# Kernel optimization log

Measured on AMD Instinct MI355X. Metric: run time of the kernel, lower is better.

The kernel has to match this reference:

```python
import jax, jax.numpy as jnp
import numpy as np

N = 50000      # nodes
E = 800000     # edges (before self-loops)
IN = 256       # input_dim
HID = 72       # hidden_dim
HEADS = 4
NEG_SLOPE = 0.2  # PyG GATConv default leaky-relu slope


def setup_inputs() -> dict:
    key = jax.random.key(0)
    ks = jax.random.split(key, 16)
    rn = lambda k, shape: jax.random.normal(k, shape, jnp.float32) * 0.05
    return {
        "x": jax.random.normal(ks[0], (N, IN), jnp.float32),
        "edge_index": jax.random.randint(ks[1], (2, E), 0, N),
        "W_in": rn(ks[2], (IN, HID)), "b_in": jnp.zeros((HID,), jnp.float32),
        "W1": rn(ks[3], (HID, HEADS * HID)),
        "a_src1": rn(ks[4], (HEADS, HID)), "a_dst1": rn(ks[5], (HEADS, HID)),
        "b1": jnp.zeros((HEADS * HID,), jnp.float32),
        "W2": rn(ks[6], (HEADS * HID, HID)),
        "a_src2": rn(ks[7], (1, HID)), "a_dst2": rn(ks[8], (1, HID)),
        "b2": jnp.zeros((HID,), jnp.float32),
        "W3": rn(ks[9], (HID, HID)),
        "a_src3": rn(ks[10], (1, HID)), "a_dst3": rn(ks[11], (1, HID)),
        "b3": jnp.zeros((HID,), jnp.float32),
        "Ws1": rn(ks[12], (HID, 32)), "bs1": jnp.zeros((32,), jnp.float32),
        "Ws2": rn(ks[13], (32, 1)), "bs2": jnp.zeros((1,), jnp.float32),
    }


def gat_conv(x, src, dst, W, a_src, a_dst, bias, concat):
    # PyG GATConv (eval mode): per-head linear, leaky-relu attention logits,
    # segment softmax over incoming edges per destination, scatter-aggregate.
    H, C = a_src.shape
    h = (x @ W).reshape(-1, H, C)                      # [N, H, C]
    logit_s = jnp.einsum('nhc,hc->nh', h, a_src)       # [N, H]
    logit_d = jnp.einsum('nhc,hc->nh', h, a_dst)       # [N, H]
    e = jax.nn.leaky_relu(logit_s[src] + logit_d[dst], NEG_SLOPE)   # [Et, H]
    emax = jax.ops.segment_max(e, dst, num_segments=N)
    emax = jnp.where(jnp.isfinite(emax), emax, 0.0)
    p = jnp.exp(e - emax[dst])
    denom = jax.ops.segment_sum(p, dst, num_segments=N)
    alpha = p / jnp.maximum(denom[dst], 1e-16)         # [Et, H]
    out = jax.ops.segment_sum(h[src] * alpha[:, :, None], dst, num_segments=N)
    out = out.reshape(-1, H * C) if concat else out.mean(axis=1)
    return out + bias


def reference(x, edge_index, W_in, b_in,
              W1, a_src1, a_dst1, b1,
              W2, a_src2, a_dst2, b2,
              W3, a_src3, a_dst3, b3,
              Ws1, bs1, Ws2, bs2):
    loops = jnp.arange(N)                              # PyG add_self_loops=True
    src = jnp.concatenate([edge_index[0], loops])
    dst = jnp.concatenate([edge_index[1], loops])
    x0 = x @ W_in + b_in                               # [N, HID]
    h = jax.nn.elu(gat_conv(x0, src, dst, W1, a_src1, a_dst1, b1, True))
    h = jax.nn.elu(gat_conv(h, src, dst, W2, a_src2, a_dst2, b2, False))
    h = jax.nn.elu(gat_conv(h, src, dst, W3, a_src3, a_dst3, b3, False))
    h = h + x0
    score = jax.nn.relu(h @ Ws1 + bs1) @ Ws2 + bs2     # dropout = identity (eval)
    return score.squeeze(-1)                           # [N]
```

## Files before the change

kernel.cpp:

```cpp
#include <hip/hip_runtime.h>
#include <hip/hip_fp16.h>
#include <cmath>

#define NN 50000
#define EE 800000
#define ET (EE + NN)
#define IN_DIM 256
#define HID 72
#define CAP 96

typedef __attribute__((ext_vector_type(8))) short s8v;
typedef __attribute__((ext_vector_type(4))) short s4v;
typedef __attribute__((ext_vector_type(4))) float f4v;
typedef __attribute__((ext_vector_type(2))) float f2v;

__device__ __forceinline__ ushort f2bf(float x) {
    uint u = __float_as_uint(x);
    return (ushort)((u + 0x7fffu + ((u >> 16) & 1u)) >> 16);
}
__device__ __forceinline__ float bf2f(ushort h) {
    return __uint_as_float(((uint)h) << 16);
}
__device__ __forceinline__ void split4(const float4& v, s4v& h, s4v& l) {
    ushort h0 = f2bf(v.x), h1 = f2bf(v.y), h2 = f2bf(v.z), h3 = f2bf(v.w);
    h = (s4v){(short)h0, (short)h1, (short)h2, (short)h3};
    l = (s4v){(short)f2bf(v.x - bf2f(h0)), (short)f2bf(v.y - bf2f(h1)),
              (short)f2bf(v.z - bf2f(h2)), (short)f2bf(v.w - bf2f(h3))};
}
__device__ __forceinline__ f4v mfma16(s8v a, s8v b, f4v c) {
    return __builtin_amdgcn_mfma_f32_16x16x32_bf16(a, b, c, 0, 0, 0);
}
__device__ __forceinline__ f2v unpack_h2(uint pv) {
    __half2 hv = __builtin_bit_cast(__half2, pv);
    return (f2v){__low2float(hv), __high2float(hv)};
}
__device__ __forceinline__ uint pack_h2(float a, float b) {
    __half2 hp = __floats2half2_rn(a, b);
    return __builtin_bit_cast(uint, hp);
}
__device__ __forceinline__ f2v fma2(float w, f2v c, f2v a) {
    return __builtin_elementwise_fma((f2v){w, w}, c, a);
}
__device__ __forceinline__ void unpack_split8(uint4 u, s8v& ah, s8v& al) {
    f2v p0 = unpack_h2(u.x), p1 = unpack_h2(u.y);
    f2v p2 = unpack_h2(u.z), p3 = unpack_h2(u.w);
    float x[8] = {p0.x, p0.y, p1.x, p1.y, p2.x, p2.y, p3.x, p3.y};
    #pragma unroll
    for (int i = 0; i < 8; ++i) {
        ushort hi = f2bf(x[i]);
        ah[i] = (short)hi;
        al[i] = (short)f2bf(x[i] - bf2f(hi));
    }
}

__device__ __forceinline__ void wsplit_one(const float* W, int ldw, int K,
        int idx, short* outH, short* outL) {
    int h = idx / (72 * K);
    int rem = idx - h * 72 * K;
    int n = rem / K, k = rem - n * K;
    float v = W[(size_t)k * ldw + h * 72 + n];
    ushort hi = f2bf(v);
    outH[idx] = (short)hi;
    outL[idx] = (short)f2bf(v - bf2f(hi));
}

#define PR0 18432
#define PR1 (PR0 + 20736)
#define PR2 (PR1 + 20736)
#define PR3 (PR2 + 5184)
#define PR4 (PR3 + 288)
#define PRTOT (PR4 + NN)

__global__ __launch_bounds__(256) void prep_kernel(
        const float* __restrict__ W_in, const float* __restrict__ W1,
        const float* __restrict__ W2, const float* __restrict__ W3,
        const float* __restrict__ a_src, const float* __restrict__ a_dst,
        short* __restrict__ BtInH, short* __restrict__ BtInL,
        short* __restrict__ Bt1H, short* __restrict__ Bt1L,
        short* __restrict__ Bt2H, short* __restrict__ Bt2L,
        short* __restrict__ Bt3H, short* __restrict__ Bt3L,
        float* __restrict__ wsrc, float* __restrict__ wdst,
        int* __restrict__ deg, ushort* __restrict__ ell) {
    int gid = blockIdx.x * 256 + threadIdx.x;
    if (gid < PR0) {
        wsplit_one(W_in, 72, 256, gid, BtInH, BtInL);
    } else if (gid < PR1) {
        wsplit_one(W1, 288, 72, gid - PR0, Bt1H, Bt1L);
    } else if (gid < PR2) {
        wsplit_one(W2, 72, 288, gid - PR1, Bt2H, Bt2L);
    } else if (gid < PR3) {
        wsplit_one(W3, 72, 72, gid - PR2, Bt3H, Bt3L);
    } else if (gid < PR4) {
        int j = gid - PR3;
        int h = j / HID, k = j % HID;
        const float* wrow = W1 + (size_t)k * (4 * HID) + h * HID;
        const float* as = a_src + h * HID;
        const float* ad = a_dst + h * HID;
        float s = 0.f, d = 0.f;
        for (int c = 0; c < HID; ++c) {
            float w = wrow[c];
            s = fmaf(w, as[c], s);
            d = fmaf(w, ad[c], d);
        }
        wsrc[j] = s;
        wdst[j] = d;
    } else if (gid < PRTOT) {
        int i = gid - PR4;
        deg[i] = 1;
        ell[(size_t)i * CAP] = (ushort)i;
    }
}

template <int NLOGIT, bool ELU_EPI, bool BATCHED, bool PACKOUT, bool APACK, bool ADJ>
__global__ __launch_bounds__(256) void gemm_mfma(
        const void* __restrict__ Ain, const short* __restrict__ BtH,
        const short* __restrict__ BtL, const float* __restrict__ bias,
        float* __restrict__ C, uint* __restrict__ Cp, int ldp,
        const float* __restrict__ lvs, const float* __restrict__ lvd,
        float* __restrict__ ls, float* __restrict__ ld,
        int M, int K, int lda, int Nfull,
        const int* __restrict__ eiw, int* __restrict__ degw,
        ushort* __restrict__ ellw, int gemmBlocks) {
    __shared__ __align__(16) short AhS[64 * 40], AlS[64 * 40];
    __shared__ __align__(16) short BhS[80 * 40], BlS[80 * 40];

    int tid = threadIdx.x;

    if (ADJ && (int)blockIdx.x >= gemmBlocks) {
        int t = (blockIdx.x - gemmBlocks) * 256 + tid;
        int i0 = t * 4;
        if (i0 < EE) {
            int4 s4 = *(const int4*)(eiw + i0);
            int4 d4 = *(const int4*)(eiw + EE + i0);
            int ss[4] = {s4.x, s4.y, s4.z, s4.w};
            int dd[4] = {d4.x, d4.y, d4.z, d4.w};
            #pragma unroll
            for (int u = 0; u < 4; ++u) {
                int pos = atomicAdd(&degw[dd[u]], 1);
                if (pos < CAP) ellw[(size_t)dd[u] * CAP + pos] = (ushort)ss[u];
            }
        }
        return;
    }

    int row0 = blockIdx.x * 64;
    int hh = BATCHED ? blockIdx.y : 0;
    int aoff = BATCHED ? hh * (APACK ? 36 : 72) : 0;
    int coff = BATCHED ? hh * 72 : 0;
    const short* bhg = BtH + (size_t)hh * 72 * K;
    const short* blg = BtL + (size_t)hh * 72 * K;

    for (int i = tid; i < 8 * 40; i += 256) {
        BhS[72 * 40 + i] = 0;
        BlS[72 * 40 + i] = 0;
    }

    int w = tid >> 6;
    int lane = tid & 63;
    int q = lane >> 4, l16 = lane & 15;

    f4v acc[5];
    #pragma unroll
    for (int f = 0; f < 5; ++f) acc[f] = (f4v)0.f;

    int ar = tid >> 2;
    int aseg = tid & 3;
    bool arok = (row0 + ar) < M;
    const float* aptrf = nullptr;
    const uint*  aptru = nullptr;
    if constexpr (APACK) {
        aptru = (const uint*)Ain + (size_t)(row0 + ar) * lda + aoff;
    } else {
        aptrf = (const float*)Ain + (size_t)(row0 + ar) * lda + aoff;
    }
    int bn0 = tid >> 2, bq0 = tid & 3;
    int bn1 = (tid + 256) >> 2;

    float4 va, vb;
    s8v bh0, bl0, bh1, bl1;
    auto gload = [&](int k0) {
        va = (float4){0, 0, 0, 0};
        vb = (float4){0, 0, 0, 0};
        int ka = k0 + aseg * 8;
        if constexpr (APACK) {
            if (arok && ka < K) {
                uint4 u = *(const uint4*)(aptru + (ka >> 1));
                f2v p0 = unpack_h2(u.x), p1 = unpack_h2(u.y);
                f2v p2 = unpack_h2(u.z), p3 = unpack_h2(u.w);
                va = (float4){p0.x, p0.y, p1.x, p1.y};
                vb = (float4){p2.x, p2.y, p3.x, p3.y};
            }
        } else {
            if (arok && ka < K)     va = *(const float4*)(aptrf + ka);
            if (arok && ka + 4 < K) vb = *(const float4*)(aptrf + ka + 4);
        }
        bh0 = (s8v)0; bl0 = (s8v)0;
        int kb = k0 + bq0 * 8;
        if (kb < K) {
            bh0 = *(const s8v*)(bhg + (size_t)bn0 * K + kb);
            bl0 = *(const s8v*)(blg + (size_t)bn0 * K + kb);
        }
        bh1 = (s8v)0; bl1 = (s8v)0;
        if (tid < 32 && kb < K) {
            bh1 = *(const s8v*)(bhg + (size_t)bn1 * K + kb);
            bl1 = *(const s8v*)(blg + (size_t)bn1 * K + kb);
        }
    };
    auto commit = [&]() {
        s4v h0, l0, h1, l1;
        split4(va, h0, l0);
        split4(vb, h1, l1);
        *(s4v*)&AhS[ar * 40 + aseg * 8]     = h0;
        *(s4v*)&AhS[ar * 40 + aseg * 8 + 4] = h1;
        *(s4v*)&AlS[ar * 40 + aseg * 8]     = l0;
        *(s4v*)&AlS[ar * 40 + aseg * 8 + 4] = l1;
        *(s8v*)&BhS[bn0 * 40 + bq0 * 8] = bh0;
        *(s8v*)&BlS[bn0 * 40 + bq0 * 8] = bl0;
        if (tid < 32) {
            *(s8v*)&BhS[bn1 * 40 + bq0 * 8] = bh1;
            *(s8v*)&BlS[bn1 * 40 + bq0 * 8] = bl1;
        }
    };

    int ntiles = (K + 31) / 32;
    gload(0);
    for (int t = 0; t < ntiles; ++t) {
        commit();
        __syncthreads();
        if (t + 1 < ntiles) gload((t + 1) * 32);
        s8v ah = *(const s8v*)&AhS[(w * 16 + l16) * 40 + q * 8];
        s8v al = *(const s8v*)&AlS[(w * 16 + l16) * 40 + q * 8];
        #pragma unroll
        for (int f = 0; f < 5; ++f) {
            s8v bh = *(const s8v*)&BhS[(f * 16 + l16) * 40 + q * 8];
            s8v bl = *(const s8v*)&BlS[(f * 16 + l16) * 40 + q * 8];
            acc[f] = mfma16(ah, bh, acc[f]);
            acc[f] = mfma16(ah, bl, acc[f]);
            acc[f] = mfma16(al, bh, acc[f]);
        }
        __syncthreads();
    }

    float v[5][4];
    #pragma unroll
    for (int f = 0; f < 5; ++f) {
        int col = f * 16 + l16;
        bool cv = col < 72;
        #pragma unroll
        for (int r = 0; r < 4; ++r) {
            float t = acc[f][r];
            if (cv && bias) t += bias[coff + col];
            if (ELU_EPI) t = (t > 0.f) ? t : expm1f(t);
            v[f][r] = cv ? t : 0.f;
        }
    }
    if (NLOGIT > 0) {
        #pragma unroll
        for (int h2 = 0; h2 < NLOGIT; ++h2) {
            #pragma unroll
            for (int r = 0; r < 4; ++r) {
                float s = 0.f, d = 0.f;
                #pragma unroll
                for (int f = 0; f < 5; ++f) {
                    int col = f * 16 + l16;
                    float lw = (col < 72) ? lvs[h2 * 72 + col] : 0.f;
                    float dw = (col < 72) ? lvd[h2 * 72 + col] : 0.f;
                    s = fmaf(v[f][r], lw, s);
                    d = fmaf(v[f][r], dw, d);
                }
                s += __shfl_xor(s, 1); s += __shfl_xor(s, 2);
                s += __shfl_xor(s, 4); s += __shfl_xor(s, 8);
                d += __shfl_xor(d, 1); d += __shfl_xor(d, 2);
                d += __shfl_xor(d, 4); d += __shfl_xor(d, 8);
                int gr = row0 + w * 16 + q * 4 + r;
                if (l16 == 0 && gr < M) {
                    ls[gr * NLOGIT + h2] = s;
                    ld[gr * NLOGIT + h2] = d;
                }
            }
        }
    }
    if (PACKOUT) {
        #pragma unroll
        for (int f = 0; f < 5; ++f) {
            int col = f * 16 + l16;
            #pragma unroll
            for (int r = 0; r < 4; ++r) {
                float vo = __shfl_xor(v[f][r], 1);
                if ((l16 & 1) == 0 && col < 72) {
                    int gr = row0 + w * 16 + q * 4 + r;
                    if (gr < M) {
                        Cp[(size_t)gr * ldp + ((coff + col) >> 1)] =
                            pack_h2(v[f][r], vo);
                    }
                }
            }
        }
    }
    if (C != nullptr) {
        #pragma unroll
        for (int f = 0; f < 5; ++f) {
            int col = f * 16 + l16;
            if (col >= 72) continue;
            #pragma unroll
            for (int r = 0; r < 4; ++r) {
                int gr = row0 + w * 16 + q * 4 + r;
                if (gr < M) C[(size_t)gr * Nfull + coff + col] = v[f][r];
            }
        }
    }
}

__global__ __launch_bounds__(256) void gemm12(
        const uint* __restrict__ a1p,
        const short* __restrict__ B1H, const short* __restrict__ B1L,
        const float* __restrict__ b1,
        const short* __restrict__ B2H, const short* __restrict__ B2L,
        const float* __restrict__ lvs, const float* __restrict__ lvd,
        float* __restrict__ lso, float* __restrict__ ldo,
        uint* __restrict__ outp) {
    __shared__ __align__(16) uint hS[64][148];
    int tid = threadIdx.x;
    int w = tid >> 6;
    int lane = tid & 63;
    int q = lane >> 4, l16 = lane & 15;
    int row0 = blockIdx.x * 64;
    int arow = w * 16 + l16;
    int gra = row0 + arow;
    bool aok = gra < NN;
    const uint* abase = a1p + (size_t)(aok ? gra : 0) * 144;

    #pragma unroll
    for (int h = 0; h < 4; ++h) {
        f4v acc[5];
        #pragma unroll
        for (int f = 0; f < 5; ++f) acc[f] = (f4v)0.f;
        #pragma unroll
        for (int t3 = 0; t3 < 3; ++t3) {
            int ks = t3 * 32 + q * 8;
            s8v ah = (s8v)0, al = (s8v)0;
            if (aok && ks < 72) {
                uint4 u = *(const uint4*)(abase + h * 36 + (ks >> 1));
                unpack_split8(u, ah, al);
            }
            #pragma unroll
            for (int f = 0; f < 5; ++f) {
                int bn = f * 16 + l16;
                s8v bh = (s8v)0, bl = (s8v)0;
                if (bn < 72 && ks < 72) {
                    bh = *(const s8v*)(B1H + ((size_t)h * 72 + bn) * 72 + ks);
                    bl = *(const s8v*)(B1L + ((size_t)h * 72 + bn) * 72 + ks);
                }
                acc[f] = mfma16(ah, bh, acc[f]);
                acc[f] = mfma16(ah, bl, acc[f]);
                acc[f] = mfma16(al, bh, acc[f]);
            }
        }
        #pragma unroll
        for (int f = 0; f < 5; ++f) {
            int col = f * 16 + l16;
            bool cv = col < 72;
            #pragma unroll
            for (int r = 0; r < 4; ++r) {
                float t = acc[f][r];
                if (cv) {
                    t += b1[h * 72 + col];
                    t = (t > 0.f) ? t : expm1f(t);
                }
                float ve = cv ? t : 0.f;
                float vo = __shfl_xor(ve, 1);
                if ((l16 & 1) == 0 && col < 72) {
                    hS[w * 16 + q * 4 + r][h * 36 + (col >> 1)] = pack_h2(ve, vo);
                }
            }
        }
    }

    f4v acc[5];
    #pragma unroll
    for (int f = 0; f < 5; ++f) acc[f] = (f4v)0.f;
    #pragma unroll
    for (int t = 0; t < 9; ++t) {
        int ks = t * 32 + q * 8;
        uint4 u = *(const uint4*)&hS[arow][ks >> 1];
        s8v ah, al;
        unpack_split8(u, ah, al);
        #pragma unroll
        for (int f = 0; f < 5; ++f) {
            int bn = f * 16 + l16;
            s8v bh = (s8v)0, bl = (s8v)0;
            if (bn < 72) {
                bh = *(const s8v*)(B2H + (size_t)bn * 288 + ks);
                bl = *(const s8v*)(B2L + (size_t)bn * 288 + ks);
            }
            acc[f] = mfma16(ah, bh, acc[f]);
            acc[f] = mfma16(ah, bl, acc[f]);
            acc[f] = mfma16(al, bh, acc[f]);
        }
    }
    float v[5][4];
    #pragma unroll
    for (int f = 0; f < 5; ++f) {
        int col = f * 16 + l16;
        bool cv = col < 72;
        #pragma unroll
        for (int r = 0; r < 4; ++r) v[f][r] = cv ? acc[f][r] : 0.f;
    }
    #pragma unroll
    for (int r = 0; r < 4; ++r) {
        float s = 0.f, d = 0.f;
        #pragma unroll
        for (int f = 0; f < 5; ++f) {
            int col = f * 16 + l16;
            float lw = (col < 72) ? lvs[col] : 0.f;
            float dw = (col < 72) ? lvd[col] : 0.f;
            s = fmaf(v[f][r], lw, s);
            d = fmaf(v[f][r], dw, d);
        }
        s += __shfl_xor(s, 1); s += __shfl_xor(s, 2);
        s += __shfl_xor(s, 4); s += __shfl_xor(s, 8);
        d += __shfl_xor(d, 1); d += __shfl_xor(d, 2);
        d += __shfl_xor(d, 4); d += __shfl_xor(d, 8);
        int gr = row0 + w * 16 + q * 4 + r;
        if (l16 == 0 && gr < NN) {
            lso[gr] = s;
            ldo[gr] = d;
        }
    }
    #pragma unroll
    for (int f = 0; f < 5; ++f) {
        int col = f * 16 + l16;
        #pragma unroll
        for (int r = 0; r < 4; ++r) {
            float vo = __shfl_xor(v[f][r], 1);
            if ((l16 & 1) == 0 && col < 72) {
                int gr = row0 + w * 16 + q * 4 + r;
                if (gr < NN) outp[(size_t)gr * 36 + (col >> 1)] = pack_h2(v[f][r], vo);
            }
        }
    }
}

template <int H, bool EPI, bool ADD_RES, bool POUT, bool SCORE>
__global__ __launch_bounds__(64) void agg_gather(
        const uint* __restrict__ featp,
        const float* __restrict__ ls, const float* __restrict__ ld,
        const int* __restrict__ degv, const ushort* __restrict__ ell,
        const float* __restrict__ bias, const float* __restrict__ res,
        float* __restrict__ out, uint* __restrict__ outp,
        const float* __restrict__ Ws1, const float* __restrict__ bs1,
        const float* __restrict__ Ws2, const float* __restrict__ bs2,
        int n) {
    __shared__ float wsh[64 * H];
    __shared__ int ssh[64];
    __shared__ float srow[HID];
    int wid = blockIdx.x;
    int lane = threadIdx.x;
    int deg = min(degv[wid], CAP);
    const ushort* row = ell + (size_t)wid * CAP;

    float ldh[H];
    if (H == 4) {
        float4 t = ((const float4*)ld)[wid];
        ldh[0] = t.x; ldh[1] = t.y; ldh[2] = t.z; ldh[3] = t.w;
    } else {
        ldh[0] = ld[wid];
    }

    f2v acc2[H];
    #pragma unroll
    for (int h = 0; h < H; ++h) acc2[h] = (f2v)0.f;

    if (deg <= 64) {
        bool act = lane < deg;
        int s = row[act ? lane : 0];
        ssh[lane] = s;
        float e[H];
        float ev[H];
        if (H == 4) {
            float4 lv = ((const float4*)ls)[s];
            ev[0] = lv.x; ev[1] = lv.y; ev[2] = lv.z; ev[3] = lv.w;
        } else {
            ev[0] = ls[s];
        }
        #pragma unroll
        for (int h = 0; h < H; ++h) {
            float vv = ev[h] + ldh[h];
            vv = (vv > 0.f) ? vv : 0.2f * vv;
            e[h] = act ? vv : -__builtin_inff();
        }
        float wv[H];
        #pragma unroll
        for (int h = 0; h < H; ++h) {
            float mh = e[h];
            #pragma unroll
            for (int off = 32; off; off >>= 1) mh = fmaxf(mh, __shfl_xor(mh, off));
            float ph = act ? expf(e[h] - mh) : 0.f;
            float sh = ph;
            #pragma unroll
            for (int off = 32; off; off >>= 1) sh += __shfl_xor(sh, off);
            wv[h] = ph / fmaxf(sh, 1e-16f);
        }
        if (H == 4) {
            ((float4*)wsh)[lane] = (float4){wv[0], wv[1], wv[2], wv[3]};
        } else {
            wsh[lane] = wv[0];
        }
        __syncthreads();

        int nb = (deg + 7) & ~7;
        const uint* rowbase = featp + (lane < 36 ? lane : 0);
        for (int t = 0; t < nb; t += 8) {
            int si[8];
            #pragma unroll
            for (int u = 0; u < 8; ++u) si[u] = ssh[t + u];
            uint pv[8];
            #pragma unroll
            for (int u = 0; u < 8; ++u) pv[u] = rowbase[(size_t)si[u] * 36];
            #pragma unroll
            for (int u = 0; u < 8; ++u) {
                f2v c2 = unpack_h2(pv[u]);
                if constexpr (H == 4) {
                    float4 we = ((const float4*)wsh)[t + u];
                    acc2[0] = fma2(we.x, c2, acc2[0]);
                    acc2[1] = fma2(we.y, c2, acc2[1]);
                    acc2[2] = fma2(we.z, c2, acc2[2]);
                    acc2[3] = fma2(we.w, c2, acc2[3]);
                } else {
                    acc2[0] = fma2(wsh[t + u], c2, acc2[0]);
                }
            }
        }
    } else {
        float m[H];
        #pragma unroll
        for (int h = 0; h < H; ++h) m[h] = -__builtin_inff();
        for (int i = lane; i < deg; i += 64) {
            int s = row[i];
            float e[H];
            if (H == 4) {
                float4 lv = ((const float4*)ls)[s];
                e[0] = lv.x; e[1] = lv.y; e[2] = lv.z; e[3] = lv.w;
            } else {
                e[0] = ls[s];
            }
            #pragma unroll
            for (int h = 0; h < H; ++h) {
                float vv = e[h] + ldh[h];
                vv = (vv > 0.f) ? vv : 0.2f * vv;
                m[h] = fmaxf(m[h], vv);
            }
        }
        #pragma unroll
        for (int h = 0; h < H; ++h)
            #pragma unroll
            for (int off = 32; off; off >>= 1) m[h] = fmaxf(m[h], __shfl_xor(m[h], off));

        float ssum[H];
        #pragma unroll
        for (int h = 0; h < H; ++h) ssum[h] = 0.f;
        for (int i = lane; i < deg; i += 64) {
            int s = row[i];
            float e[H];
            if (H == 4) {
                float4 lv = ((const float4*)ls)[s];
                e[0] = lv.x; e[1] = lv.y; e[2] = lv.z; e[3] = lv.w;
            } else {
                e[0] = ls[s];
            }
            #pragma unroll
            for (int h = 0; h < H; ++h) {
                float vv = e[h] + ldh[h];
                vv = (vv > 0.f) ? vv : 0.2f * vv;
                ssum[h] += expf(vv - m[h]);
            }
        }
        #pragma unroll
        for (int h = 0; h < H; ++h)
            #pragma unroll
            for (int off = 32; off; off >>= 1) ssum[h] += __shfl_xor(ssum[h], off);
        float inv[H];
        #pragma unroll
        for (int h = 0; h < H; ++h) inv[h] = 1.f / fmaxf(ssum[h], 1e-16f);

        for (int base = 0; base < deg; base += 64) {
            int i = base + lane;
            int lim = min(64, deg - base);
            if (i < deg) {
                int s = row[i];
                ssh[lane] = s;
                float e[H];
                if (H == 4) {
                    float4 lv = ((const float4*)ls)[s];
                    e[0] = lv.x; e[1] = lv.y; e[2] = lv.z; e[3] = lv.w;
                } else {
                    e[0] = ls[s];
                }
                if (H == 4) {
                    float p0 = expf(((e[0] + ldh[0] > 0.f) ? e[0] + ldh[0] : 0.2f * (e[0] + ldh[0])) - m[0]) * inv[0];
                    float p1 = expf(((e[1] + ldh[1] > 0.f) ? e[1] + ldh[1] : 0.2f * (e[1] + ldh[1])) - m[1]) * inv[1];
                    float p2 = expf(((e[2] + ldh[2] > 0.f) ? e[2] + ldh[2] : 0.2f * (e[2] + ldh[2])) - m[2]) * inv[2];
                    float p3 = expf(((e[3] + ldh[3] > 0.f) ? e[3] + ldh[3] : 0.2f * (e[3] + ldh[3])) - m[3]) * inv[3];
                    ((float4*)wsh)[lane] = (float4){p0, p1, p2, p3};
                } else {
                    float vv = e[0] + ldh[0];
                    vv = (vv > 0.f) ? vv : 0.2f * vv;
                    wsh[lane] = expf(vv - m[0]) * inv[0];
                }
            }
            __syncthreads();
            for (int t = 0; t < lim; ++t) {
                uint pv = featp[(size_t)ssh[t] * 36 + (lane < 36 ? lane : 0)];
                f2v c2 = unpack_h2(pv);
                if constexpr (H == 4) {
                    float4 we = ((const float4*)wsh)[t];
                    acc2[0] = fma2(we.x, c2, acc2[0]);
                    acc2[1] = fma2(we.y, c2, acc2[1]);
                    acc2[2] = fma2(we.z, c2, acc2[2]);
                    acc2[3] = fma2(we.w, c2, acc2[3]);
                } else {
                    acc2[0] = fma2(wsh[t], c2, acc2[0]);
                }
            }
            __syncthreads();
        }
    }

    if (lane < 36) {
        #pragma unroll
        for (int h = 0; h < H; ++h) {
            float v0 = acc2[h].x, v1 = acc2[h].y;
            if (EPI) {
                v0 += bias[2 * lane];
                v1 += bias[2 * lane + 1];
                v0 = (v0 > 0.f) ? v0 : expm1f(v0);
                v1 = (v1 > 0.f) ? v1 : expm1f(v1);
                if (ADD_RES) {
                    float2 rr = *(const float2*)&res[(size_t)wid * HID + 2 * lane];
                    v0 += rr.x; v1 += rr.y;
                }
            }
            if (POUT) {
                outp[(size_t)wid * (H * 36) + h * 36 + lane] = pack_h2(v0, v1);
            } else if (SCORE) {
                srow[2 * lane] = v0;
                srow[2 * lane + 1] = v1;
            } else {
                *(float2*)&out[(size_t)wid * (H * HID) + h * HID + 2 * lane] =
                    (float2){v0, v1};
            }
        }
    }
    if (SCORE) {
        __syncthreads();
        if (lane < 32) {
            float acc = bs1[lane];
            #pragma unroll 8
            for (int c = 0; c < HID; ++c)
                acc = fmaf(srow[c], Ws1[c * 32 + lane], acc);
            float v = fmaxf(acc, 0.f) * Ws2[lane];
            #pragma unroll
            for (int off = 16; off; off >>= 1) v += __shfl_down(v, off, 32);
            if (lane == 0) out[wid] = v + bs2[0];
        }
    }
}

extern "C" void kernel_launch(void* const* d_in, const int* in_sizes, int n_in,
                              void* d_out, int out_size, void* d_ws, size_t ws_size,
                              hipStream_t stream) {
    const float* x      = (const float*)d_in[0];
    const int*   ei     = (const int*)  d_in[1];
    const float* W_in   = (const float*)d_in[2];
    const float* b_in   = (const float*)d_in[3];
    const float* W1     = (const float*)d_in[4];
    const float* a_src1 = (const float*)d_in[5];
    const float* a_dst1 = (const float*)d_in[6];
    const float* b1     = (const float*)d_in[7];
    const float* W2     = (const float*)d_in[8];
    const float* a_src2 = (const float*)d_in[9];
    const float* a_dst2 = (const float*)d_in[10];
    const float* b2     = (const float*)d_in[11];
    const float* W3     = (const float*)d_in[12];
    const float* a_src3 = (const float*)d_in[13];
    const float* a_dst3 = (const float*)d_in[14];
    const float* b3     = (const float*)d_in[15];
    const float* Ws1    = (const float*)d_in[16];
    const float* bs1    = (const float*)d_in[17];
    const float* Ws2    = (const float*)d_in[18];
    const float* bs2    = (const float*)d_in[19];
    float* out = (float*)d_out;

    float* ws    = (float*)d_ws;
    float* x0    = ws;
    float* ls    = x0 + (size_t)NN * HID;
    float* ld    = ls + (size_t)NN * 4;
    float* ls3   = ld + (size_t)NN * 4;
    float* ld3   = ls3 + NN;
    float* wsrc1 = ld3 + NN;
    float* wdst1 = wsrc1 + 288;
    int* deg     = (int*)(wdst1 + 288);
    ushort* ell  = (ushort*)(deg + NN);
    uintptr_t bp = ((uintptr_t)(ell + (size_t)NN * CAP) + 15) & ~(uintptr_t)15;
    short* BtInH = (short*)bp;
    short* BtInL = BtInH + 18432;
    short* Bt1H  = BtInL + 18432;
    short* Bt1L  = Bt1H + 20736;
    short* Bt2H  = Bt1L + 20736;
    short* Bt2L  = Bt2H + 20736;
    short* Bt3H  = Bt2L + 20736;
    short* Bt3L  = Bt3H + 5184;
    uint*  x0p   = (uint*)(Bt3L + 5184);
    uint*  a1p   = x0p + (size_t)NN * 36;
    uint*  hp2p  = a1p + (size_t)NN * 144;
    uint*  h2p   = hp2p + (size_t)NN * 36;
    uint*  hp3p  = h2p + (size_t)NN * 36;

    prep_kernel<<<(PRTOT + 255) / 256, 256, 0, stream>>>(
        W_in, W1, W2, W3, a_src1, a_dst1,
        BtInH, BtInL, Bt1H, Bt1L, Bt2H, Bt2L, Bt3H, Bt3L, wsrc1, wdst1,
        deg, ell);

    const int mblocks = (NN + 63) / 64;
    const int adjBlocks = (EE / 4 + 255) / 256;
    gemm_mfma<4, false, false, true, false, true>
        <<<dim3(mblocks + adjBlocks, 1), 256, 0, stream>>>(
        x, BtInH, BtInL, b_in, x0, x0p, 36, wsrc1, wdst1, ls, ld,
        NN, IN_DIM, IN_DIM, HID, ei, deg, ell, mblocks);
    agg_gather<4, false, false, true, false><<<NN, 64, 0, stream>>>(
        x0p, ls, ld, deg, ell, nullptr, nullptr, nullptr, a1p,
        nullptr, nullptr, nullptr, nullptr, NN);
    gemm12<<<mblocks, 256, 0, stream>>>(
        a1p, Bt1H, Bt1L, b1, Bt2H, Bt2L, a_src2, a_dst2, ls, ld, hp2p);
    agg_gather<1, true, false, true, false><<<NN, 64, 0, stream>>>(
        hp2p, ls, ld, deg, ell, b2, nullptr, nullptr, h2p,
        nullptr, nullptr, nullptr, nullptr, NN);
    gemm_mfma<1, false, false, true, true, false><<<dim3(mblocks, 1), 256, 0, stream>>>(
        h2p, Bt3H, Bt3L, nullptr, nullptr, hp3p, 36, a_src3, a_dst3, ls3, ld3,
        NN, HID, 36, 0, nullptr, nullptr, nullptr, 0);
    agg_gather<1, true, true, false, true><<<NN, 64, 0, stream>>>(
        hp3p, ls3, ld3, deg, ell, b3, x0, out, nullptr,
        Ws1, bs1, Ws2, bs2, NN);
}
```

Baseline: 368.4 us.

## Eliminate layer-3 GEMM by aggregating before projecting and folding logits

Drops the separate layer-3 MFMA GEMM kernel. Layer-3 attention logits are now computed in the layer-2 aggregation epilogue as dot products of h2 with W3·a_src3 and W3·a_dst3, which are precomputed in the prep kernel. The final aggregation gathers h2 directly and applies W3 per node after aggregation, using linearity, and then adds bias, ELU, the residual and the score head. This removes one kernel launch and an intermediate buffer write and read, but adds a per-node 72x72 fp32 matvec to the last gather kernel, reading W3 from global memory.

```diff
diff --git a/kernel.cpp b/kernel.cpp
--- a/kernel.cpp
+++ b/kernel.cpp
@@ -67,19 +67,20 @@
 #define PR0 18432
 #define PR1 (PR0 + 20736)
 #define PR2 (PR1 + 20736)
-#define PR3 (PR2 + 5184)
-#define PR4 (PR3 + 288)
+#define PR3 (PR2 + 288)
+#define PR4 (PR3 + 144)
 #define PRTOT (PR4 + NN)
 
 __global__ __launch_bounds__(256) void prep_kernel(
         const float* __restrict__ W_in, const float* __restrict__ W1,
         const float* __restrict__ W2, const float* __restrict__ W3,
         const float* __restrict__ a_src, const float* __restrict__ a_dst,
+        const float* __restrict__ a_src3, const float* __restrict__ a_dst3,
         short* __restrict__ BtInH, short* __restrict__ BtInL,
         short* __restrict__ Bt1H, short* __restrict__ Bt1L,
         short* __restrict__ Bt2H, short* __restrict__ Bt2L,
-        short* __restrict__ Bt3H, short* __restrict__ Bt3L,
         float* __restrict__ wsrc, float* __restrict__ wdst,
+        float* __restrict__ w3s, float* __restrict__ w3d,
         int* __restrict__ deg, ushort* __restrict__ ell) {
     int gid = blockIdx.x * 256 + threadIdx.x;
     if (gid < PR0) {
@@ -89,9 +90,7 @@
     } else if (gid < PR2) {
         wsplit_one(W2, 72, 288, gid - PR1, Bt2H, Bt2L);
     } else if (gid < PR3) {
-        wsplit_one(W3, 72, 72, gid - PR2, Bt3H, Bt3L);
-    } else if (gid < PR4) {
-        int j = gid - PR3;
+        int j = gid - PR2;
         int h = j / HID, k = j % HID;
         const float* wrow = W1 + (size_t)k * (4 * HID) + h * HID;
         const float* as = a_src + h * HID;
@@ -104,6 +103,14 @@
         }
         wsrc[j] = s;
         wdst[j] = d;
+    } else if (gid < PR4) {
+        int j = gid - PR3;
+        int c = (j < 72) ? j : j - 72;
+        const float* a3 = (j < 72) ? a_src3 : a_dst3;
+        const float* wrow = W3 + (size_t)c * HID;
+        float acc = 0.f;
+        for (int o = 0; o < HID; ++o) acc = fmaf(wrow[o], a3[o], acc);
+        if (j < 72) w3s[c] = acc; else w3d[c] = acc;
     } else if (gid < PRTOT) {
         int i = gid - PR4;
         deg[i] = 1;
@@ -441,19 +448,23 @@
     }
 }
 
-template <int H, bool EPI, bool ADD_RES, bool POUT, bool SCORE>
+template <int H, bool EPI, bool ADD_RES, bool POUT, bool SCORE, bool L3OUT>
 __global__ __launch_bounds__(64) void agg_gather(
         const uint* __restrict__ featp,
         const float* __restrict__ ls, const float* __restrict__ ld,
         const int* __restrict__ degv, const ushort* __restrict__ ell,
         const float* __restrict__ bias, const float* __restrict__ res,
         float* __restrict__ out, uint* __restrict__ outp,
+        const float* __restrict__ w3s, const float* __restrict__ w3d,
+        float* __restrict__ ls3, float* __restrict__ ld3,
+        const float* __restrict__ W3g,
         const float* __restrict__ Ws1, const float* __restrict__ bs1,
         const float* __restrict__ Ws2, const float* __restrict__ bs2,
         int n) {
     __shared__ float wsh[64 * H];
     __shared__ int ssh[64];
     __shared__ float srow[HID];
+    __shared__ float gsh[HID];
     int wid = blockIdx.x;
     int lane = threadIdx.x;
     int deg = min(degv[wid], CAP);
@@ -626,32 +637,72 @@
         }
     }
 
-    if (lane < 36) {
-        #pragma unroll
-        for (int h = 0; h < H; ++h) {
-            float v0 = acc2[h].x, v1 = acc2[h].y;
-            if (EPI) {
-                v0 += bias[2 * lane];
-                v1 += bias[2 * lane + 1];
-                v0 = (v0 > 0.f) ? v0 : expm1f(v0);
-                v1 = (v1 > 0.f) ? v1 : expm1f(v1);
-                if (ADD_RES) {
-                    float2 rr = *(const float2*)&res[(size_t)wid * HID + 2 * lane];
-                    v0 += rr.x; v1 += rr.y;
-                }
-            }
-            if (POUT) {
-                outp[(size_t)wid * (H * 36) + h * 36 + lane] = pack_h2(v0, v1);
-            } else if (SCORE) {
-                srow[2 * lane] = v0;
-                srow[2 * lane + 1] = v1;
-            } else {
-                *(float2*)&out[(size_t)wid * (H * HID) + h * HID + 2 * lane] =
-                    (float2){v0, v1};
-            }
-        }
-    }
-    if (SCORE) {
+    if (!SCORE) {
+        float ev0 = 0.f, ev1 = 0.f;
+        if (lane < 36) {
+            #pragma unroll
+            for (int h = 0; h < H; ++h) {
+                float v0 = acc2[h].x, v1 = acc2[h].y;
+                if (EPI) {
+                    v0 += bias[2 * lane];
+                    v1 += bias[2 * lane + 1];
+                    v0 = (v0 > 0.f) ? v0 : expm1f(v0);
+                    v1 = (v1 > 0.f) ? v1 : expm1f(v1);
+                    if (ADD_RES) {
+                        float2 rr = *(const float2*)&res[(size_t)wid * HID + 2 * lane];
+                        v0 += rr.x; v1 += rr.y;
+                    }
+                }
+                if (POUT) {
+                    outp[(size_t)wid * (H * 36) + h * 36 + lane] = pack_h2(v0, v1);
+                } else {
+                    *(float2*)&out[(size_t)wid * (H * HID) + h * HID + 2 * lane] =
+                        (float2){v0, v1};
+                }
+                if (L3OUT && H == 1) { ev0 = v0; ev1 = v1; }
+            }
+        }
+        if (L3OUT) {
+            float s = 0.f, d = 0.f;
+            if (lane < 36) {
+                float2 as = *(const float2*)&w3s[2 * lane];
+                float2 ad = *(const float2*)&w3d[2 * lane];
+                s = ev0 * as.x + ev1 * as.y;
+                d = ev0 * ad.x + ev1 * ad.y;
+            }
+            #pragma unroll
+            for (int off = 32; off; off >>= 1) {
+                s += __shfl_xor(s, off);
+                d += __shfl_xor(d, off);
+            }
+            if (lane == 0) {
+                ls3[wid] = s;
+                ld3[wid] = d;
+            }
+        }
+    } else {
+        if (lane < 36) {
+            gsh[2 * lane] = acc2[0].x;
+            gsh[2 * lane + 1] = acc2[0].y;
+        }
+        __syncthreads();
+        if (lane < 36) {
+            float t0 = 0.f, t1 = 0.f;
+            #pragma unroll 8
+            for (int c = 0; c < HID; ++c) {
+                float g = gsh[c];
+                float2 wv = *(const float2*)&W3g[(size_t)c * HID + 2 * lane];
+                t0 = fmaf(g, wv.x, t0);
+                t1 = fmaf(g, wv.y, t1);
+            }
+            t0 += bias[2 * lane];
+            t1 += bias[2 * lane + 1];
+            t0 = (t0 > 0.f) ? t0 : expm1f(t0);
+            t1 = (t1 > 0.f) ? t1 : expm1f(t1);
+            float2 rr = *(const float2*)&res[(size_t)wid * HID + 2 * lane];
+            srow[2 * lane] = t0 + rr.x;
+            srow[2 * lane + 1] = t1 + rr.y;
+        }
         __syncthreads();
         if (lane < 32) {
             float acc = bs1[lane];
@@ -699,7 +750,9 @@
     float* ld3   = ls3 + NN;
     float* wsrc1 = ld3 + NN;
     float* wdst1 = wsrc1 + 288;
-    int* deg     = (int*)(wdst1 + 288);
+    float* w3s   = wdst1 + 288;
+    float* w3d   = w3s + 72;
+    int* deg     = (int*)(w3d + 72);
     ushort* ell  = (ushort*)(deg + NN);
     uintptr_t bp = ((uintptr_t)(ell + (size_t)NN * CAP) + 15) & ~(uintptr_t)15;
     short* BtInH = (short*)bp;
@@ -708,17 +761,14 @@
     short* Bt1L  = Bt1H + 20736;
     short* Bt2H  = Bt1L + 20736;
     short* Bt2L  = Bt2H + 20736;
-    short* Bt3H  = Bt2L + 20736;
-    short* Bt3L  = Bt3H + 5184;
-    uint*  x0p   = (uint*)(Bt3L + 5184);
+    uint*  x0p   = (uint*)(Bt2L + 20736);
     uint*  a1p   = x0p + (size_t)NN * 36;
     uint*  hp2p  = a1p + (size_t)NN * 144;
     uint*  h2p   = hp2p + (size_t)NN * 36;
-    uint*  hp3p  = h2p + (size_t)NN * 36;
 
     prep_kernel<<<(PRTOT + 255) / 256, 256, 0, stream>>>(
-        W_in, W1, W2, W3, a_src1, a_dst1,
-        BtInH, BtInL, Bt1H, Bt1L, Bt2H, Bt2L, Bt3H, Bt3L, wsrc1, wdst1,
+        W_in, W1, W2, W3, a_src1, a_dst1, a_src3, a_dst3,
+        BtInH, BtInL, Bt1H, Bt1L, Bt2H, Bt2L, wsrc1, wdst1, w3s, w3d,
         deg, ell);
 
     const int mblocks = (NN + 63) / 64;
@@ -727,18 +777,18 @@
         <<<dim3(mblocks + adjBlocks, 1), 256, 0, stream>>>(
         x, BtInH, BtInL, b_in, x0, x0p, 36, wsrc1, wdst1, ls, ld,
         NN, IN_DIM, IN_DIM, HID, ei, deg, ell, mblocks);
-    agg_gather<4, false, false, true, false><<<NN, 64, 0, stream>>>(
+    agg_gather<4, false, false, true, false, false><<<NN, 64, 0, stream>>>(
         x0p, ls, ld, deg, ell, nullptr, nullptr, nullptr, a1p,
+        nullptr, nullptr, nullptr, nullptr, nullptr,
         nullptr, nullptr, nullptr, nullptr, NN);
     gemm12<<<mblocks, 256, 0, stream>>>(
         a1p, Bt1H, Bt1L, b1, Bt2H, Bt2L, a_src2, a_dst2, ls, ld, hp2p);
-    agg_gather<1, true, false, true, false><<<NN, 64, 0, stream>>>(
+    agg_gather<1, true, false, true, false, true><<<NN, 64, 0, stream>>>(
         hp2p, ls, ld, deg, ell, b2, nullptr, nullptr, h2p,
+        w3s, w3d, ls3, ld3, nullptr,
         nullptr, nullptr, nullptr, nullptr, NN);
-    gemm_mfma<1, false, false, true, true, false><<<dim3(mblocks, 1), 256, 0, stream>>>(
-        h2p, Bt3H, Bt3L, nullptr, nullptr, hp3p, 36, a_src3, a_dst3, ls3, ld3,
-        NN, HID, 36, 0, nullptr, nullptr, nullptr, 0);
-    agg_gather<1, true, true, false, true><<<NN, 64, 0, stream>>>(
-        hp3p, ls3, ld3, deg, ell, b3, x0, out, nullptr,
+    agg_gather<1, false, true, false, true, false><<<NN, 64, 0, stream>>>(
+        h2p, ls3, ld3, deg, ell, b3, x0, out, nullptr,
+        nullptr, nullptr, nullptr, nullptr, W3,
         Ws1, bs1, Ws2, bs2, NN);
 }
```

After: 447.4 us. 21.4% more time.
